# Optimization experiments

Hardware: AMD Instinct MI355X
Metric: run time of the kernel (lower is better)

Reference implementation:

```python
import jax, jax.numpy as jnp
import numpy as np

BATCH_SIZE = 2048
TEMPERATURE = 0.5
EPS = 1e-8  # torch CosineSimilarity eps


def setup_inputs() -> dict:
    key = jax.random.key(0)
    k1, k2 = jax.random.split(key)
    d = 512
    z_i = jax.random.normal(k1, (BATCH_SIZE, d), dtype=jnp.float32)
    z_j = jax.random.normal(k2, (BATCH_SIZE, d), dtype=jnp.float32)
    return {"z_i": z_i, "z_j": z_j}


def reference(z_i, z_j):
    B = BATCH_SIZE
    n = 2 * B
    z = jnp.concatenate([z_i, z_j], axis=0)              # [n, d]
    # cosine similarity via normalize + GEMM (same math as broadcasted CosineSimilarity)
    norms = jnp.maximum(jnp.linalg.norm(z, axis=1, keepdims=True), EPS)
    zn = z / norms                                       # [n, d]
    S = zn @ zn.T                                        # [n, n]
    # drop diagonal: row i keeps columns j != i, in order (matches sim[~eye].view(n, n-1))
    cols = jnp.arange(n - 1)[None, :]                    # [1, n-1]
    rows = jnp.arange(n)[:, None]                        # [n, 1]
    idx = cols + (cols >= rows)                          # skip diagonal
    off_diag = jnp.take_along_axis(S, idx, axis=1)       # [n, n-1]
    # positive pair: pos_pairs = cat(z_j, z_i) -> partner index (i + B) mod n
    pos = jnp.take_along_axis(S, ((rows[:, 0] + B) % n)[:, None], axis=1)  # [n, 1]
    logits = jnp.concatenate([pos, off_diag], axis=1) / TEMPERATURE        # [n, n]
    # cross-entropy with label 0, reduction='sum', then / n  == mean over rows
    loss = jnp.mean(jax.nn.logsumexp(logits, axis=1) - logits[:, 0])
    return loss
```

## Files before the change

kernel.cpp:

```cpp
#include <hip/hip_runtime.h>
#include <hip/hip_bf16.h>

#define N_TOT 4096
#define D     512
#define BHALF 2048

#define EXP2_SCALE 2.8853900817779268f
#define E2 7.3890560989306495f

typedef __attribute__((ext_vector_type(4))) float floatx4;

#define AS_GLOBAL(p) ((const __attribute__((address_space(1))) void*)(p))
#define AS_LDS(p)    ((__attribute__((address_space(3))) void*)(p))

#define WAITCNT_VM(n) (0xF70 | (n))

__global__ void normalize_kernel(const float* __restrict__ z_i,
                                 const float* __restrict__ z_j,
                                 unsigned char* __restrict__ zn,
                                 float* __restrict__ rowsum) {
    const int wave = threadIdx.x >> 6, lane = threadIdx.x & 63;
    const int row = blockIdx.x * 4 + wave;
    const float* src = (row < BHALF) ? (z_i + (size_t)row * D)
                                     : (z_j + (size_t)(row - BHALF) * D);
    if (lane == 0) rowsum[row] = 0.0f;
    float4 v0 = ((const float4*)src)[lane];
    float4 v1 = ((const float4*)src)[lane + 64];
    float ss = v0.x*v0.x + v0.y*v0.y + v0.z*v0.z + v0.w*v0.w
             + v1.x*v1.x + v1.y*v1.y + v1.z*v1.z + v1.w*v1.w;
    #pragma unroll
    for (int off = 32; off > 0; off >>= 1) ss += __shfl_xor(ss, off);
    float inv = 1.0f / fmaxf(sqrtf(ss), 1e-8f);
    int w0 = __builtin_amdgcn_cvt_pk_fp8_f32(v0.x * inv, v0.y * inv, 0, false);
    w0     = __builtin_amdgcn_cvt_pk_fp8_f32(v0.z * inv, v0.w * inv, w0, true);
    int w1 = __builtin_amdgcn_cvt_pk_fp8_f32(v1.x * inv, v1.y * inv, 0, false);
    w1     = __builtin_amdgcn_cvt_pk_fp8_f32(v1.z * inv, v1.w * inv, w1, true);
    int* dst = (int*)(zn + (size_t)row * D);
    dst[lane]      = w0;
    dst[lane + 64] = w1;
}

__launch_bounds__(256)
__global__ void gemm_fused(const unsigned char* __restrict__ zn,
                           float* __restrict__ rowsum,
                           float* __restrict__ spos) {
    __shared__ unsigned char At[3][128 * 32];
    __shared__ unsigned char Bt[3][128 * 32];

    int b = blockIdx.x, bi = 0, rowlen = 32;
    while (b >= rowlen) { b -= rowlen; rowlen--; bi++; }
    const int bj = bi + b;
    const int i0 = bi * 128;
    const int j0 = bj * 128;

    const int t = threadIdx.x;
    const int lane = t & 63, wave = t >> 6;
    const int wm = wave & 1, wn = wave >> 1;
    const int quad = lane >> 4, l16 = lane & 15;

    const int srow = wave * 32 + (lane >> 1);
    const int scol = (lane & 1) * 16;
    const unsigned char* gA = zn + (size_t)(i0 + srow) * D + scol;
    const unsigned char* gB = zn + (size_t)(j0 + srow) * D + scol;
    const int lo = srow * 32 + scol;

    floatx4 acc[4][4] = {};

    __builtin_amdgcn_global_load_lds(AS_GLOBAL(gA),      AS_LDS(&At[0][lo]), 16, 0, 0);
    __builtin_amdgcn_global_load_lds(AS_GLOBAL(gB),      AS_LDS(&Bt[0][lo]), 16, 0, 0);
    __builtin_amdgcn_global_load_lds(AS_GLOBAL(gA + 32), AS_LDS(&At[1][lo]), 16, 0, 0);
    __builtin_amdgcn_global_load_lds(AS_GLOBAL(gB + 32), AS_LDS(&Bt[1][lo]), 16, 0, 0);

    #pragma unroll
    for (int kt = 0; kt < 16; ++kt) {
        const int cur = kt % 3;
        if (kt < 15) __builtin_amdgcn_s_waitcnt(WAITCNT_VM(2));
        else         __builtin_amdgcn_s_waitcnt(WAITCNT_VM(0));
        __builtin_amdgcn_s_barrier();
        __asm__ volatile("" ::: "memory");
        if (kt < 14) {
            const int nxt = (kt + 2) % 3;
            const int ko = (kt + 2) * 32;
            __builtin_amdgcn_global_load_lds(AS_GLOBAL(gA + ko), AS_LDS(&At[nxt][lo]), 16, 0, 0);
            __builtin_amdgcn_global_load_lds(AS_GLOBAL(gB + ko), AS_LDS(&Bt[nxt][lo]), 16, 0, 0);
        }
        long af[4], bf[4];
        #pragma unroll
        for (int tm = 0; tm < 4; ++tm)
            af[tm] = *(const long*)(&At[cur][(wm*64 + tm*16 + l16) * 32 + quad*8]);
        #pragma unroll
        for (int tn = 0; tn < 4; ++tn)
            bf[tn] = *(const long*)(&Bt[cur][(wn*64 + tn*16 + l16) * 32 + quad*8]);
        #pragma unroll
        for (int tm = 0; tm < 4; ++tm)
            #pragma unroll
            for (int tn = 0; tn < 4; ++tn)
                acc[tm][tn] = __builtin_amdgcn_mfma_f32_16x16x32_fp8_fp8(
                    af[tm], bf[tn], acc[tm][tn], 0, 0, 0);
    }

    float cs[4] = {0.f, 0.f, 0.f, 0.f};
    #pragma unroll
    for (int tm = 0; tm < 4; ++tm) {
        float rs[4] = {0.f, 0.f, 0.f, 0.f};
        #pragma unroll
        for (int tn = 0; tn < 4; ++tn)
            #pragma unroll
            for (int r = 0; r < 4; ++r) {
                float e = exp2f(acc[tm][tn][r] * EXP2_SCALE);
                rs[r] += e;
                cs[tn] += e;
            }
        #pragma unroll
        for (int r = 0; r < 4; ++r) {
            float v = rs[r];
            v += __shfl_xor(v, 1);
            v += __shfl_xor(v, 2);
            v += __shfl_xor(v, 4);
            v += __shfl_xor(v, 8);
            if (l16 == 0) {
                int gi = i0 + wm*64 + tm*16 + quad*4 + r;
                atomicAdd(&rowsum[gi], v);
            }
        }
    }
    if (bi != bj) {
        #pragma unroll
        for (int tn = 0; tn < 4; ++tn) {
            float v = cs[tn];
            v += __shfl_xor(v, 16);
            v += __shfl_xor(v, 32);
            if (quad == 0) {
                int gj = j0 + wn*64 + tn*16 + l16;
                atomicAdd(&rowsum[gj], v);
            }
        }
    }
    if (bj == bi + 16) {
        #pragma unroll
        for (int tm = 0; tm < 4; ++tm)
            #pragma unroll
            for (int tn = 0; tn < 4; ++tn)
                #pragma unroll
                for (int r = 0; r < 4; ++r) {
                    int li = wm*64 + tm*16 + quad*4 + r;
                    int lj = wn*64 + tn*16 + l16;
                    if (li == lj) {
                        float s = acc[tm][tn][r];
                        spos[i0 + li]         = s;
                        spos[i0 + li + BHALF] = s;
                    }
                }
    }
}

__global__ void finalize_kernel(const float* __restrict__ rowsum,
                                const float* __restrict__ spos,
                                float* __restrict__ out) {
    int t = threadIdx.x;
    float acc = 0.f;
    for (int i = t; i < N_TOT; i += 1024) {
        float sp = spos[i];
        float denom = rowsum[i] - E2 + exp2f(sp * EXP2_SCALE);
        acc += __logf(denom) - 2.0f * sp;
    }
    #pragma unroll
    for (int off = 32; off > 0; off >>= 1) acc += __shfl_xor(acc, off);
    __shared__ float red[16];
    if ((t & 63) == 0) red[t >> 6] = acc;
    __syncthreads();
    if (t == 0) {
        float s = 0.f;
        #pragma unroll
        for (int w = 0; w < 16; ++w) s += red[w];
        out[0] = s / (float)N_TOT;
    }
}

extern "C" void kernel_launch(void* const* d_in, const int* in_sizes, int n_in,
                              void* d_out, int out_size, void* d_ws, size_t ws_size,
                              hipStream_t stream) {
    const float* z_i = (const float*)d_in[0];
    const float* z_j = (const float*)d_in[1];
    float* out = (float*)d_out;

    char* ws = (char*)d_ws;
    unsigned char* zn = (unsigned char*)ws;
    float* rowsum = (float*)(ws + (size_t)N_TOT * D);
    float* spos   = rowsum + N_TOT;

    normalize_kernel<<<N_TOT / 4, 256, 0, stream>>>(z_i, z_j, zn, rowsum);
    gemm_fused<<<(32 * 33) / 2, 256, 0, stream>>>(zn, rowsum, spos);
    finalize_kernel<<<1, 1024, 0, stream>>>(rowsum, spos, out);
}
```

Baseline: 89.35 us.

## Give each wave private LDS staging to drop block barriers in GEMM loop

Each wave now loads its own A and B 64-row slices into a private LDS region, so the per-iteration block barrier is removed and waves run their k-loops independently. This doubles global-to-LDS traffic per block, since A and B slices are loaded redundantly by the two waves that share them. The change also adds s_setprio around the MFMA burst and an occupancy hint of 3 blocks per CU. LDS use grows from 24KB to 48KB per block.

```diff
diff --git a/kernel.cpp b/kernel.cpp
--- a/kernel.cpp
+++ b/kernel.cpp
@@ -40,12 +40,11 @@
     dst[lane + 64] = w1;
 }
 
-__launch_bounds__(256)
+__launch_bounds__(256, 3)
 __global__ void gemm_fused(const unsigned char* __restrict__ zn,
                            float* __restrict__ rowsum,
                            float* __restrict__ spos) {
-    __shared__ unsigned char At[3][128 * 32];
-    __shared__ unsigned char Bt[3][128 * 32];
+    __shared__ unsigned char L[3][4][2][2048];
 
     int b = blockIdx.x, bi = 0, rowlen = 32;
     while (b >= rowlen) { b -= rowlen; rowlen--; bi++; }
@@ -58,46 +57,51 @@
     const int wm = wave & 1, wn = wave >> 1;
     const int quad = lane >> 4, l16 = lane & 15;
 
-    const int srow = wave * 32 + (lane >> 1);
+    const int srow = lane >> 1;
     const int scol = (lane & 1) * 16;
-    const unsigned char* gA = zn + (size_t)(i0 + srow) * D + scol;
-    const unsigned char* gB = zn + (size_t)(j0 + srow) * D + scol;
-    const int lo = srow * 32 + scol;
+    const unsigned char* gA = zn + (size_t)(i0 + wm * 64 + srow) * D + scol;
+    const unsigned char* gB = zn + (size_t)(j0 + wn * 64 + srow) * D + scol;
+
+#define STAGE(bufidx, ko) do {                                                               \
+    __builtin_amdgcn_global_load_lds(AS_GLOBAL(gA + (ko)),                                   \
+        AS_LDS(&L[bufidx][wave][0][lane * 16]),        16, 0, 0);                            \
+    __builtin_amdgcn_global_load_lds(AS_GLOBAL(gA + (ko) + 32 * D),                          \
+        AS_LDS(&L[bufidx][wave][0][1024 + lane * 16]), 16, 0, 0);                            \
+    __builtin_amdgcn_global_load_lds(AS_GLOBAL(gB + (ko)),                                   \
+        AS_LDS(&L[bufidx][wave][1][lane * 16]),        16, 0, 0);                            \
+    __builtin_amdgcn_global_load_lds(AS_GLOBAL(gB + (ko) + 32 * D),                          \
+        AS_LDS(&L[bufidx][wave][1][1024 + lane * 16]), 16, 0, 0);                            \
+} while (0)
 
     floatx4 acc[4][4] = {};
 
-    __builtin_amdgcn_global_load_lds(AS_GLOBAL(gA),      AS_LDS(&At[0][lo]), 16, 0, 0);
-    __builtin_amdgcn_global_load_lds(AS_GLOBAL(gB),      AS_LDS(&Bt[0][lo]), 16, 0, 0);
-    __builtin_amdgcn_global_load_lds(AS_GLOBAL(gA + 32), AS_LDS(&At[1][lo]), 16, 0, 0);
-    __builtin_amdgcn_global_load_lds(AS_GLOBAL(gB + 32), AS_LDS(&Bt[1][lo]), 16, 0, 0);
+    STAGE(0, 0);
+    STAGE(1, 32);
 
     #pragma unroll
     for (int kt = 0; kt < 16; ++kt) {
         const int cur = kt % 3;
-        if (kt < 15) __builtin_amdgcn_s_waitcnt(WAITCNT_VM(2));
+        if (kt < 15) __builtin_amdgcn_s_waitcnt(WAITCNT_VM(4));
         else         __builtin_amdgcn_s_waitcnt(WAITCNT_VM(0));
-        __builtin_amdgcn_s_barrier();
         __asm__ volatile("" ::: "memory");
-        if (kt < 14) {
-            const int nxt = (kt + 2) % 3;
-            const int ko = (kt + 2) * 32;
-            __builtin_amdgcn_global_load_lds(AS_GLOBAL(gA + ko), AS_LDS(&At[nxt][lo]), 16, 0, 0);
-            __builtin_amdgcn_global_load_lds(AS_GLOBAL(gB + ko), AS_LDS(&Bt[nxt][lo]), 16, 0, 0);
-        }
+        if (kt < 14) STAGE((kt + 2) % 3, (kt + 2) * 32);
         long af[4], bf[4];
         #pragma unroll
         for (int tm = 0; tm < 4; ++tm)
-            af[tm] = *(const long*)(&At[cur][(wm*64 + tm*16 + l16) * 32 + quad*8]);
+            af[tm] = *(const long*)(&L[cur][wave][0][(tm * 16 + l16) * 32 + quad * 8]);
         #pragma unroll
         for (int tn = 0; tn < 4; ++tn)
-            bf[tn] = *(const long*)(&Bt[cur][(wn*64 + tn*16 + l16) * 32 + quad*8]);
+            bf[tn] = *(const long*)(&L[cur][wave][1][(tn * 16 + l16) * 32 + quad * 8]);
+        __builtin_amdgcn_s_setprio(1);
         #pragma unroll
         for (int tm = 0; tm < 4; ++tm)
             #pragma unroll
             for (int tn = 0; tn < 4; ++tn)
                 acc[tm][tn] = __builtin_amdgcn_mfma_f32_16x16x32_fp8_fp8(
                     af[tm], bf[tn], acc[tm][tn], 0, 0, 0);
+        __builtin_amdgcn_s_setprio(0);
     }
+#undef STAGE
 
     float cs[4] = {0.f, 0.f, 0.f, 0.f};
     #pragma unroll
```

Result: no change. 88.87 us (-0.5%).
